# Kernel optimization log

Measured on AMD Instinct MI355X. Metric: run time of the kernel, lower is better.

The kernel has to match this reference:

```python
import jax, jax.numpy as jnp
import numpy as np

ALPHA = 1.702   # SwiGLU alpha
LIMIT = 7.0     # swiglu_limit clamp
EPS = 1e-5      # RMSNorm eps
TOPK = 4        # experts_per_token
CHUNK = 8       # token chunk for gathered-weight einsum (bounds memory)


def _swiglu(h):
    # h: (..., 2*I) with interleaved [glu, linear] pairs
    g = jnp.minimum(h[..., ::2], LIMIT)
    l = jnp.clip(h[..., 1::2], -LIMIT, LIMIT)
    return g * jax.nn.sigmoid(ALPHA * g) * (l + 1.0)


def setup_inputs() -> dict:
    key = jax.random.key(0)
    ks = jax.random.split(key, 5)
    T, H, I, E = 1024, 1024, 1024, 64
    s = 0.02
    return {
        "x": jax.random.normal(ks[0], (T, H), jnp.float32),
        "norm_scale": jnp.ones((H,), jnp.float32),
        "gate_w": jax.random.normal(ks[1], (E, H), jnp.float32) * s,
        "gate_b": jnp.zeros((E,), jnp.float32),
        "mlp1_w": jax.random.normal(ks[2], (E, 2 * I, H), jnp.float32) * s,
        "mlp1_b": jnp.zeros((E, 2 * I), jnp.float32),
        "mlp2_w": jax.random.normal(ks[3], (E, H, I), jnp.float32) * s,
        "mlp2_b": jnp.zeros((E, H), jnp.float32),
    }


def reference(x, norm_scale, gate_w, gate_b, mlp1_w, mlp1_b, mlp2_w, mlp2_b):
    # RMSNorm (fp32 math)
    t = x * jax.lax.rsqrt(jnp.mean(x * x, axis=-1, keepdims=True) + EPS) * norm_scale
    # gating: top-k over gate logits, softmax over the k selected
    logits = t @ gate_w.T + gate_b                     # (T, E)
    vals, idx = jax.lax.top_k(logits, TOPK)            # sorted desc, matches torch.topk(sorted=True)
    ew = jax.nn.softmax(vals, axis=-1)                 # (T, k)

    T_, H = t.shape
    nc = T_ // CHUNK

    @jax.checkpoint
    def per_chunk(args):
        xc, ic, wc = args                              # (C,H), (C,k), (C,k)
        h = jnp.einsum('bekh,bh->bek', mlp1_w[ic], xc) + mlp1_b[ic]   # (C,k,2I)
        h = _swiglu(h)                                                 # (C,k,I)
        o = jnp.einsum('behi,bei->beh', mlp2_w[ic], h) + mlp2_b[ic]    # (C,k,H)
        return jnp.einsum('beh,be->bh', o, wc)                         # (C,H)

    out = jax.lax.map(per_chunk, (t.reshape(nc, CHUNK, H),
                                  idx.reshape(nc, CHUNK, TOPK),
                                  ew.reshape(nc, CHUNK, TOPK)))
    return x + out.reshape(T_, H)
```

## Files before the change

### kernel.cpp

```cpp
#include <hip/hip_runtime.h>
#include <hip/hip_bf16.h>

#define GLOBAL_AS __attribute__((address_space(1)))
#define LDS_AS    __attribute__((address_space(3)))

typedef __bf16 bf16x8 __attribute__((ext_vector_type(8)));
typedef __bf16 bf16x4 __attribute__((ext_vector_type(4)));
typedef float  f32x4v __attribute__((ext_vector_type(4)));

__global__ __launch_bounds__(256) void k_rmsnorm(const float* __restrict__ x,
        const float* __restrict__ sc, float* __restrict__ t32,
        __bf16* __restrict__ t16)
{
    const int t = blockIdx.x, tid = threadIdx.x;
    const float4 v = ((const float4*)(x + (size_t)t * 1024))[tid];
    float ss = v.x*v.x + v.y*v.y + v.z*v.z + v.w*v.w;
    #pragma unroll
    for (int s = 32; s; s >>= 1) ss += __shfl_xor(ss, s, 64);
    __shared__ float red[4];
    if ((tid & 63) == 0) red[tid >> 6] = ss;
    __syncthreads();
    const float tot = red[0] + red[1] + red[2] + red[3];
    const float rs = rsqrtf(tot * (1.0f / 1024.0f) + 1e-5f);
    const float4 s4 = ((const float4*)sc)[tid];
    float4 o;
    o.x = v.x * rs * s4.x; o.y = v.y * rs * s4.y;
    o.z = v.z * rs * s4.z; o.w = v.w * rs * s4.w;
    ((float4*)(t32 + (size_t)t * 1024))[tid] = o;
    bf16x4 p;
    p[0] = (__bf16)o.x; p[1] = (__bf16)o.y; p[2] = (__bf16)o.z; p[3] = (__bf16)o.w;
    ((bf16x4*)(t16 + (size_t)t * 1024))[tid] = p;
}

__global__ __launch_bounds__(256) void k_gate(const float* __restrict__ t32,
        const float* __restrict__ gw, const float* __restrict__ gb,
        int* __restrict__ idx, float* __restrict__ ew)
{
    const int t = blockIdx.x, tid = threadIdx.x;
    __shared__ float4 tl[256];
    __shared__ float part[4][64];
    tl[tid] = ((const float4*)(t32 + (size_t)t * 1024))[tid];
    __syncthreads();
    const int q = tid >> 6, e = tid & 63;
    const float4* w4 = (const float4*)(gw + (size_t)e * 1024 + q * 256);
    const float4* a4 = &tl[q * 64];
    float acc = 0.0f;
    #pragma unroll 8
    for (int i = 0; i < 64; ++i) {
        const float4 a = a4[i], b = w4[i];
        acc += a.x*b.x + a.y*b.y + a.z*b.z + a.w*b.w;
    }
    part[q][e] = acc;
    __syncthreads();
    if (tid < 64) {
        float cur = part[0][tid] + part[1][tid] + part[2][tid] + part[3][tid] + gb[tid];
        float vals[4]; int ids[4];
        #pragma unroll
        for (int k = 0; k < 4; ++k) {
            float m = cur;
            #pragma unroll
            for (int s = 32; s; s >>= 1) m = fmaxf(m, __shfl_xor(m, s, 64));
            const unsigned long long b = __ballot(cur == m);
            const int bi = __ffsll(b) - 1;
            vals[k] = m; ids[k] = bi;
            if (tid == bi) cur = -3.0e38f;
        }
        float ex[4], s = 0.0f;
        #pragma unroll
        for (int k = 0; k < 4; ++k) { ex[k] = expf(vals[k] - vals[0]); s += ex[k]; }
        if (tid < 4) { idx[t * 4 + tid] = ids[tid]; ew[t * 4 + tid] = ex[tid] / s; }
    }
}

__global__ __launch_bounds__(256) void k_bucket(const int* __restrict__ idx,
        const float* __restrict__ ewv, int* __restrict__ eoff,
        int* __restrict__ slot_token, float* __restrict__ slot_ew,
        int* __restrict__ token_slots)
{
    __shared__ int cnt[64], cur[64];
    const int tid = threadIdx.x;
    if (tid < 64) cnt[tid] = 0;
    __syncthreads();
    for (int p = tid; p < 4096; p += 256) atomicAdd(&cnt[idx[p]], 1);
    __syncthreads();
    if (tid == 0) {
        int s = 0;
        for (int e = 0; e < 64; ++e) { eoff[e] = s; cur[e] = s; s += cnt[e]; }
        eoff[64] = s;
    }
    __syncthreads();
    for (int p = tid; p < 4096; p += 256) {
        const int e = idx[p];
        const int s = atomicAdd(&cur[e], 1);
        slot_token[s] = p >> 2;
        slot_ew[s] = ewv[p];
        token_slots[p] = s;
    }
}

template<int MODE>
__global__ __launch_bounds__(256, 4) void k_gemm(
        const float* __restrict__ W, const float* __restrict__ Bias,
        const __bf16* __restrict__ A,
        const int* __restrict__ eoff, const int* __restrict__ slot_token,
        const float* __restrict__ slot_ew,
        __bf16* __restrict__ act_out, __bf16* __restrict__ o_buf)
{
    constexpr int NPE = (MODE == 0) ? 2048 : 1024;
    const int e  = blockIdx.y;
    const int nt = blockIdx.x;
    const int off = eoff[e];
    const int count = eoff[e + 1] - off;
    if (count == 0) return;
    const int tid = threadIdx.x;
    const int wv = tid >> 6, l = tid & 63;
    const int wm = wv >> 1, wn = wv & 1;

    __shared__ __attribute__((aligned(16))) unsigned char lds_a[2][16384];
    __shared__ __attribute__((aligned(16))) unsigned char lds_b[8192];

    const float* Wb = W + (size_t)e * NPE * 1024 + (size_t)nt * 64 * 1024;

#define DMA_A(sbuf, kt) do {                                                   \
    _Pragma("unroll")                                                          \
    for (int i_ = 0; i_ < 4; ++i_)                                             \
        __builtin_amdgcn_global_load_lds(                                      \
            (const GLOBAL_AS void*)(asrc[i_] + (kt) * 128),                    \
            (LDS_AS void*)&lds_a[sbuf][(wv * 4 + i_) * 1024], 16, 0, 0);       \
    } while (0)

#define LOAD_B(dst, kt) do {                                                   \
    _Pragma("unroll")                                                          \
    for (int it_ = 0; it_ < 4; ++it_) {                                        \
        const int fid_ = it_ * 256 + tid;                                      \
        dst[it_] = *(const float4*)(Wb + (size_t)(fid_ >> 4) * 1024            \
                                    + (kt) * 64 + (fid_ & 15) * 4);            \
    } } while (0)

#define WRITE_B(src) do {                                                      \
    _Pragma("unroll")                                                          \
    for (int it_ = 0; it_ < 4; ++it_) {                                        \
        const int fid_ = it_ * 256 + tid;                                      \
        const int row_ = fid_ >> 4, c4_ = fid_ & 15;                           \
        bf16x4 p_;                                                             \
        p_[0] = (__bf16)src[it_].x; p_[1] = (__bf16)src[it_].y;                \
        p_[2] = (__bf16)src[it_].z; p_[3] = (__bf16)src[it_].w;                \
        *(bf16x4*)(&lds_b[row_ * 128 +                                         \
                   ((c4_ * 8) ^ ((row_ & 7) << 4))]) = p_;                     \
    } } while (0)

#define COMPUTE(cbuf) do {                                                     \
    _Pragma("unroll")                                                          \
    for (int kk_ = 0; kk_ < 2; ++kk_) {                                        \
        bf16x8 af_[4], bf_[2];                                                 \
        _Pragma("unroll")                                                      \
        for (int m_ = 0; m_ < 4; ++m_) {                                       \
            const int row_ = wm * 64 + m_ * 16 + (l & 15);                     \
            af_[m_] = *(const bf16x8*)(&lds_a[cbuf][row_ * 128 +               \
                      ((kk_ * 64 + ((l >> 4) * 16)) ^ ((row_ & 7) << 4))]);    \
        }                                                                      \
        _Pragma("unroll")                                                      \
        for (int n_ = 0; n_ < 2; ++n_) {                                       \
            const int row_ = wn * 32 + n_ * 16 + (l & 15);                     \
            bf_[n_] = *(const bf16x8*)(&lds_b[row_ * 128 +                     \
                      ((kk_ * 64 + ((l >> 4) * 16)) ^ ((row_ & 7) << 4))]);    \
        }                                                                      \
        _Pragma("unroll")                                                      \
        for (int m_ = 0; m_ < 4; ++m_)                                         \
            _Pragma("unroll")                                                  \
            for (int n_ = 0; n_ < 2; ++n_)                                     \
                acc[m_][n_] = __builtin_amdgcn_mfma_f32_16x16x32_bf16(         \
                                  af_[m_], bf_[n_], acc[m_][n_], 0, 0, 0);     \
    } } while (0)

#define VMC(n)  asm volatile("s_waitcnt vmcnt(" #n ")" ::: "memory")
#define LGKM0() asm volatile("s_waitcnt lgkmcnt(0)" ::: "memory")
#define SB()    __builtin_amdgcn_sched_barrier(0)
#define BAR()   __builtin_amdgcn_s_barrier()

    for (int mt = 0; mt * 128 < count; ++mt) {
        const unsigned char* asrc[4];
        #pragma unroll
        for (int i = 0; i < 4; ++i) {
            const int chunk = wv * 4 + i;
            const int row = chunk * 8 + (l >> 3);
            const int colbyte = ((l & 7) ^ (l >> 3)) << 4;
            int arow;
            if (MODE == 0) {
                int slot = off + mt * 128 + row;
                const int smax = off + count - 1;
                if (slot > smax) slot = smax;
                arow = slot_token[slot];
            } else {
                arow = off + mt * 128 + row;
            }
            asrc[i] = (const unsigned char*)A + (size_t)arow * 2048 + colbyte;
        }

        f32x4v acc[4][2];
        #pragma unroll
        for (int m = 0; m < 4; ++m)
            #pragma unroll
            for (int n = 0; n < 2; ++n)
                acc[m][n] = f32x4v{0.f, 0.f, 0.f, 0.f};

        float4 bvA[4], bvB[4];

        DMA_A(0, 0); SB(); LOAD_B(bvA, 0); SB();
        DMA_A(1, 1); SB(); LOAD_B(bvB, 1); SB();
        VMC(8);
        WRITE_B(bvA); LGKM0(); SB(); BAR();
        COMPUTE(0); BAR();

        #pragma unroll 1
        for (int p = 0; p < 7; ++p) {
            DMA_A(0, 2 * p + 2); SB(); LOAD_B(bvA, 2 * p + 2); SB();
            VMC(8);
            WRITE_B(bvB); LGKM0(); SB(); BAR();
            COMPUTE(1); BAR();
            DMA_A(1, 2 * p + 3); SB(); LOAD_B(bvB, 2 * p + 3); SB();
            VMC(8);
            WRITE_B(bvA); LGKM0(); SB(); BAR();
            COMPUTE(0); BAR();
        }

        VMC(0);
        WRITE_B(bvB); LGKM0(); SB(); BAR();
        COMPUTE(1);

        #pragma unroll
        for (int m = 0; m < 4; ++m) {
            #pragma unroll
            for (int n = 0; n < 2; ++n) {
                #pragma unroll
                for (int j = 0; j < 4; ++j) {
                    const int row  = wm * 64 + m * 16 + (l >> 4) * 4 + j;
                    const int coll = wn * 32 + n * 16 + (l & 15);
                    const int gn = nt * 64 + coll;
                    const int gm = mt * 128 + row;
                    if (MODE == 0) {
                        float v = acc[m][n][j] + Bias[(size_t)e * NPE + gn];
                        const float partner = __shfl_xor(v, 1, 64);
                        if (!(l & 1) && gm < count) {
                            const float g  = fminf(v, 7.0f);
                            const float lv = fminf(fmaxf(partner, -7.0f), 7.0f);
                            const float r  = g / (1.0f + expf(-1.702f * g)) * (lv + 1.0f);
                            act_out[(size_t)(off + gm) * 1024 + (gn >> 1)] = (__bf16)r;
                        }
                    } else {
                        if (gm < count) {
                            const int slot = off + gm;
                            const float v = acc[m][n][j] + Bias[(size_t)e * NPE + gn];
                            o_buf[(size_t)slot * 1024 + gn] = (__bf16)(v * slot_ew[slot]);
                        }
                    }
                }
            }
        }
        BAR();
    }
#undef DMA_A
#undef LOAD_B
#undef WRITE_B
#undef COMPUTE
#undef VMC
#undef LGKM0
#undef SB
#undef BAR
}

__global__ __launch_bounds__(256) void k_combine(const float* __restrict__ x,
        const __bf16* __restrict__ o_buf, const int* __restrict__ tslot,
        float* __restrict__ out)
{
    const int t = blockIdx.x, tid = threadIdx.x;
    float4 r = ((const float4*)(x + (size_t)t * 1024))[tid];
    #pragma unroll
    for (int k = 0; k < 4; ++k) {
        const int s = tslot[t * 4 + k];
        const bf16x4 o = ((const bf16x4*)(o_buf + (size_t)s * 1024))[tid];
        r.x += (float)o[0]; r.y += (float)o[1];
        r.z += (float)o[2]; r.w += (float)o[3];
    }
    ((float4*)(out + (size_t)t * 1024))[tid] = r;
}

extern "C" void kernel_launch(void* const* d_in, const int* in_sizes, int n_in,
                              void* d_out, int out_size, void* d_ws, size_t ws_size,
                              hipStream_t stream)
{
    const float* x   = (const float*)d_in[0];
    const float* nsc = (const float*)d_in[1];
    const float* gw  = (const float*)d_in[2];
    const float* gb  = (const float*)d_in[3];
    const float* w1  = (const float*)d_in[4];
    const float* b1  = (const float*)d_in[5];
    const float* w2  = (const float*)d_in[6];
    const float* b2  = (const float*)d_in[7];
    float* out = (float*)d_out;
    (void)in_sizes; (void)n_in; (void)out_size; (void)ws_size;

    char* ws = (char*)d_ws;
    float*  t32   = (float*)(ws);
    __bf16* t16   = (__bf16*)(ws + (4u  << 20));
    __bf16* act   = (__bf16*)(ws + (6u  << 20));
    __bf16* obuf  = (__bf16*)(ws + (16u << 20));
    int*    idx   = (int*)  (ws + (34u << 20));
    float*  ew    = (float*)(ws + (34u << 20) + 1 * 65536);
    int*    stok  = (int*)  (ws + (34u << 20) + 2 * 65536);
    float*  sew   = (float*)(ws + (34u << 20) + 3 * 65536);
    int*    tslot = (int*)  (ws + (34u << 20) + 4 * 65536);
    int*    eoff  = (int*)  (ws + (34u << 20) + 5 * 65536);

    k_rmsnorm<<<1024, 256, 0, stream>>>(x, nsc, t32, t16);
    k_gate   <<<1024, 256, 0, stream>>>(t32, gw, gb, idx, ew);
    k_bucket <<<   1, 256, 0, stream>>>(idx, ew, eoff, stok, sew, tslot);
    k_gemm<0><<<dim3(32, 64), 256, 0, stream>>>(w1, b1, t16, eoff, stok, sew, act, nullptr);
    k_gemm<1><<<dim3(16, 64), 256, 0, stream>>>(w2, b2, act, eoff, stok, sew, nullptr, obuf);
    k_combine<<<1024, 256, 0, stream>>>(x, obuf, tslot, out);
}
```

Before: 289.1 us.

## Widen N tiles, shrink M tiles to 96, remap expert grid order

Retiles both expert GEMMs to 96-row M tiles and wider N tiles (256 for mlp1, 128 for mlp2), so each fp32 weight tile is read and converted by fewer blocks and fewer rows are wasted at the ends of expert buckets. The K loop is restructured to one register buffer with loads issued right after compute, and the flattened grid index is remapped to interleave experts across the launch. The cost is fewer, larger blocks (occupancy hint drops from 4 to 2) and more registers per thread, which may reduce latency hiding.

```diff
diff --git a/kernel.cpp b/kernel.cpp
--- a/kernel.cpp
+++ b/kernel.cpp
@@ -99,7 +99,7 @@
 }
 
 template<int MODE>
-__global__ __launch_bounds__(256, 4) void k_gemm(
+__global__ __launch_bounds__(256, 2) void k_gemm(
         const float* __restrict__ W, const float* __restrict__ Bias,
         const __bf16* __restrict__ A,
         const int* __restrict__ eoff, const int* __restrict__ slot_token,
@@ -107,44 +107,49 @@
         __bf16* __restrict__ act_out, __bf16* __restrict__ o_buf)
 {
     constexpr int NPE = (MODE == 0) ? 2048 : 1024;
-    const int e  = blockIdx.y;
-    const int nt = blockIdx.x;
+    constexpr int BN  = (MODE == 0) ?  256 :  128;
+    constexpr int NIT = BN / 16;
+    constexpr int NF  = BN / 32;
+    const int d  = blockIdx.y * gridDim.x + blockIdx.x;
+    const int e  = (d & 7) * 8 + ((d >> 3) & 7);
+    const int nt = d >> 6;
     const int off = eoff[e];
     const int count = eoff[e + 1] - off;
     if (count == 0) return;
     const int tid = threadIdx.x;
     const int wv = tid >> 6, l = tid & 63;
     const int wm = wv >> 1, wn = wv & 1;
-
-    __shared__ __attribute__((aligned(16))) unsigned char lds_a[2][16384];
-    __shared__ __attribute__((aligned(16))) unsigned char lds_b[8192];
-
-    const float* Wb = W + (size_t)e * NPE * 1024 + (size_t)nt * 64 * 1024;
+    const int lrow = l & 15, lq = l >> 4;
+
+    __shared__ __attribute__((aligned(16))) unsigned char lds_a[2][12288];
+    __shared__ __attribute__((aligned(16))) unsigned char lds_b[BN * 128];
+
+    const float* Wb = W + ((size_t)e * NPE + (size_t)nt * BN) * 1024;
 
 #define DMA_A(sbuf, kt) do {                                                   \
     _Pragma("unroll")                                                          \
-    for (int i_ = 0; i_ < 4; ++i_)                                             \
+    for (int i_ = 0; i_ < 3; ++i_)                                             \
         __builtin_amdgcn_global_load_lds(                                      \
             (const GLOBAL_AS void*)(asrc[i_] + (kt) * 128),                    \
-            (LDS_AS void*)&lds_a[sbuf][(wv * 4 + i_) * 1024], 16, 0, 0);       \
+            (LDS_AS void*)&lds_a[sbuf][(wv * 3 + i_) * 1024], 16, 0, 0);       \
     } while (0)
 
-#define LOAD_B(dst, kt) do {                                                   \
+#define LOAD_B(kt) do {                                                        \
     _Pragma("unroll")                                                          \
-    for (int it_ = 0; it_ < 4; ++it_) {                                        \
+    for (int it_ = 0; it_ < NIT; ++it_) {                                      \
         const int fid_ = it_ * 256 + tid;                                      \
-        dst[it_] = *(const float4*)(Wb + (size_t)(fid_ >> 4) * 1024            \
-                                    + (kt) * 64 + (fid_ & 15) * 4);            \
+        bv[it_] = *(const float4*)(Wb + (size_t)(fid_ >> 4) * 1024             \
+                                   + (kt) * 64 + (fid_ & 15) * 4);             \
     } } while (0)
 
-#define WRITE_B(src) do {                                                      \
+#define WRITE_B() do {                                                         \
     _Pragma("unroll")                                                          \
-    for (int it_ = 0; it_ < 4; ++it_) {                                        \
+    for (int it_ = 0; it_ < NIT; ++it_) {                                      \
         const int fid_ = it_ * 256 + tid;                                      \
         const int row_ = fid_ >> 4, c4_ = fid_ & 15;                           \
         bf16x4 p_;                                                             \
-        p_[0] = (__bf16)src[it_].x; p_[1] = (__bf16)src[it_].y;                \
-        p_[2] = (__bf16)src[it_].z; p_[3] = (__bf16)src[it_].w;                \
+        p_[0] = (__bf16)bv[it_].x; p_[1] = (__bf16)bv[it_].y;                  \
+        p_[2] = (__bf16)bv[it_].z; p_[3] = (__bf16)bv[it_].w;                  \
         *(bf16x4*)(&lds_b[row_ * 128 +                                         \
                    ((c4_ * 8) ^ ((row_ & 7) << 4))]) = p_;                     \
     } } while (0)
@@ -152,92 +157,90 @@
 #define COMPUTE(cbuf) do {                                                     \
     _Pragma("unroll")                                                          \
     for (int kk_ = 0; kk_ < 2; ++kk_) {                                        \
-        bf16x8 af_[4], bf_[2];                                                 \
+        bf16x8 af_[3], bf_[NF];                                                \
         _Pragma("unroll")                                                      \
-        for (int m_ = 0; m_ < 4; ++m_) {                                       \
-            const int row_ = wm * 64 + m_ * 16 + (l & 15);                     \
+        for (int m_ = 0; m_ < 3; ++m_) {                                       \
+            const int row_ = wm * 48 + m_ * 16 + lrow;                         \
             af_[m_] = *(const bf16x8*)(&lds_a[cbuf][row_ * 128 +               \
-                      ((kk_ * 64 + ((l >> 4) * 16)) ^ ((row_ & 7) << 4))]);    \
+                      ((kk_ * 64 + lq * 16) ^ ((row_ & 7) << 4))]);            \
         }                                                                      \
         _Pragma("unroll")                                                      \
-        for (int n_ = 0; n_ < 2; ++n_) {                                       \
-            const int row_ = wn * 32 + n_ * 16 + (l & 15);                     \
+        for (int n_ = 0; n_ < NF; ++n_) {                                      \
+            const int row_ = wn * (BN / 2) + n_ * 16 + lrow;                   \
             bf_[n_] = *(const bf16x8*)(&lds_b[row_ * 128 +                     \
-                      ((kk_ * 64 + ((l >> 4) * 16)) ^ ((row_ & 7) << 4))]);    \
+                      ((kk_ * 64 + lq * 16) ^ ((row_ & 7) << 4))]);            \
         }                                                                      \
         _Pragma("unroll")                                                      \
-        for (int m_ = 0; m_ < 4; ++m_)                                         \
+        for (int m_ = 0; m_ < 3; ++m_)                                         \
             _Pragma("unroll")                                                  \
-            for (int n_ = 0; n_ < 2; ++n_)                                     \
+            for (int n_ = 0; n_ < NF; ++n_)                                    \
                 acc[m_][n_] = __builtin_amdgcn_mfma_f32_16x16x32_bf16(         \
                                   af_[m_], bf_[n_], acc[m_][n_], 0, 0, 0);     \
     } } while (0)
 
-#define VMC(n)  asm volatile("s_waitcnt vmcnt(" #n ")" ::: "memory")
+#define VMC0()  asm volatile("s_waitcnt vmcnt(0)" ::: "memory")
 #define LGKM0() asm volatile("s_waitcnt lgkmcnt(0)" ::: "memory")
 #define SB()    __builtin_amdgcn_sched_barrier(0)
 #define BAR()   __builtin_amdgcn_s_barrier()
 
-    for (int mt = 0; mt * 128 < count; ++mt) {
-        const unsigned char* asrc[4];
-        #pragma unroll
-        for (int i = 0; i < 4; ++i) {
-            const int chunk = wv * 4 + i;
+    const int nmt = (count + 95) / 96;
+    for (int mt = 0; mt < nmt; ++mt) {
+        const unsigned char* asrc[3];
+        #pragma unroll
+        for (int i = 0; i < 3; ++i) {
+            const int chunk = wv * 3 + i;
             const int row = chunk * 8 + (l >> 3);
             const int colbyte = ((l & 7) ^ (l >> 3)) << 4;
             int arow;
             if (MODE == 0) {
-                int slot = off + mt * 128 + row;
+                int slot = off + mt * 96 + row;
                 const int smax = off + count - 1;
                 if (slot > smax) slot = smax;
                 arow = slot_token[slot];
             } else {
-                arow = off + mt * 128 + row;
+                arow = off + mt * 96 + row;
             }
             asrc[i] = (const unsigned char*)A + (size_t)arow * 2048 + colbyte;
         }
 
-        f32x4v acc[4][2];
-        #pragma unroll
-        for (int m = 0; m < 4; ++m)
+        f32x4v acc[3][NF];
+        #pragma unroll
+        for (int m = 0; m < 3; ++m)
             #pragma unroll
-            for (int n = 0; n < 2; ++n)
+            for (int n = 0; n < NF; ++n)
                 acc[m][n] = f32x4v{0.f, 0.f, 0.f, 0.f};
 
-        float4 bvA[4], bvB[4];
-
-        DMA_A(0, 0); SB(); LOAD_B(bvA, 0); SB();
-        DMA_A(1, 1); SB(); LOAD_B(bvB, 1); SB();
-        VMC(8);
-        WRITE_B(bvA); LGKM0(); SB(); BAR();
-        COMPUTE(0); BAR();
+        float4 bv[NIT];
+
+        DMA_A(0, 0); SB();
+        LOAD_B(0);
+        WRITE_B();
+        VMC0(); LGKM0(); SB(); BAR(); SB();
+        DMA_A(1, 1); SB();
+        LOAD_B(1); SB();
 
         #pragma unroll 1
-        for (int p = 0; p < 7; ++p) {
-            DMA_A(0, 2 * p + 2); SB(); LOAD_B(bvA, 2 * p + 2); SB();
-            VMC(8);
-            WRITE_B(bvB); LGKM0(); SB(); BAR();
-            COMPUTE(1); BAR();
-            DMA_A(1, 2 * p + 3); SB(); LOAD_B(bvB, 2 * p + 3); SB();
-            VMC(8);
-            WRITE_B(bvA); LGKM0(); SB(); BAR();
-            COMPUTE(0); BAR();
+        for (int kt = 0; kt < 16; ++kt) {
+            COMPUTE(kt & 1);
+            if (kt == 15) break;
+            BAR(); SB();
+            WRITE_B();
+            if (kt < 14) {
+                DMA_A(kt & 1, kt + 2); SB();
+                LOAD_B(kt + 2);
+            }
+            LGKM0(); SB(); BAR(); SB();
         }
 
-        VMC(0);
-        WRITE_B(bvB); LGKM0(); SB(); BAR();
-        COMPUTE(1);
-
-        #pragma unroll
-        for (int m = 0; m < 4; ++m) {
+        #pragma unroll
+        for (int m = 0; m < 3; ++m) {
             #pragma unroll
-            for (int n = 0; n < 2; ++n) {
+            for (int n = 0; n < NF; ++n) {
                 #pragma unroll
                 for (int j = 0; j < 4; ++j) {
-                    const int row  = wm * 64 + m * 16 + (l >> 4) * 4 + j;
-                    const int coll = wn * 32 + n * 16 + (l & 15);
-                    const int gn = nt * 64 + coll;
-                    const int gm = mt * 128 + row;
+                    const int row = wm * 48 + m * 16 + lq * 4 + j;
+                    const int gn = nt * BN + wn * (BN / 2) + n * 16 + lrow;
+                    const int gm = mt * 96 + row;
                     if (MODE == 0) {
                         float v = acc[m][n][j] + Bias[(size_t)e * NPE + gn];
                         const float partner = __shfl_xor(v, 1, 64);
@@ -249,9 +252,9 @@
                         }
                     } else {
                         if (gm < count) {
-                            const int slot = off + gm;
+                            const int sl = off + gm;
                             const float v = acc[m][n][j] + Bias[(size_t)e * NPE + gn];
-                            o_buf[(size_t)slot * 1024 + gn] = (__bf16)(v * slot_ew[slot]);
+                            o_buf[(size_t)sl * 1024 + gn] = (__bf16)(v * slot_ew[sl]);
                         }
                     }
                 }
@@ -263,7 +266,7 @@
 #undef LOAD_B
 #undef WRITE_B
 #undef COMPUTE
-#undef VMC
+#undef VMC0
 #undef LGKM0
 #undef SB
 #undef BAR
@@ -315,7 +318,7 @@
     k_rmsnorm<<<1024, 256, 0, stream>>>(x, nsc, t32, t16);
     k_gate   <<<1024, 256, 0, stream>>>(t32, gw, gb, idx, ew);
     k_bucket <<<   1, 256, 0, stream>>>(idx, ew, eoff, stok, sew, tslot);
-    k_gemm<0><<<dim3(32, 64), 256, 0, stream>>>(w1, b1, t16, eoff, stok, sew, act, nullptr);
-    k_gemm<1><<<dim3(16, 64), 256, 0, stream>>>(w2, b2, act, eoff, stok, sew, nullptr, obuf);
+    k_gemm<0><<<dim3(8, 64), 256, 0, stream>>>(w1, b1, t16, eoff, stok, sew, act, nullptr);
+    k_gemm<1><<<dim3(8, 64), 256, 0, stream>>>(w2, b2, act, eoff, stok, sew, nullptr, obuf);
     k_combine<<<1024, 256, 0, stream>>>(x, obuf, tslot, out);
 }
```

Result: slower. 302.1 us (+4.5%).
